# Optimization experiments

Hardware: AMD Instinct MI355X
Metric: run time of the kernel (lower is better)

Reference implementation:

```python
import jax, jax.numpy as jnp
import numpy as np

B, S, E, H = 2, 2048, 1024, 16
D = E // H


def setup_inputs() -> dict:
    key = jax.random.key(0)
    ks = jax.random.split(key, 8)
    q = jax.random.normal(ks[0], (B, S, E), dtype=jnp.float32)
    k = jax.random.normal(ks[1], (B, S, E), dtype=jnp.float32)
    v = jax.random.normal(ks[2], (B, S, E), dtype=jnp.float32)
    mask = jax.random.randint(ks[3], (B, 1, 1, S), 0, 2, dtype=jnp.int32)
    sc = 1.0 / np.sqrt(E)
    W_qkv = jax.random.normal(ks[4], (3 * E, E), dtype=jnp.float32) * sc
    b_qkv = jnp.zeros((3 * E,), dtype=jnp.float32)
    W_out = jax.random.normal(ks[5], (E, E), dtype=jnp.float32) * sc
    b_out = jnp.zeros((E,), dtype=jnp.float32)
    return {"q": q, "k": k, "v": v, "mask": mask,
            "W_qkv": W_qkv, "b_qkv": b_qkv, "W_out": W_out, "b_out": b_out}


def reference(q, k, v, mask, W_qkv, b_qkv, W_out, b_out):
    # Fused qkv linear: q takes the Q-slice, k the K-slice, v the V-slice.
    qp = (q @ W_qkv[:E].T + b_qkv[:E]).reshape(B, S, H, D)
    kp = (k @ W_qkv[E:2 * E].T + b_qkv[E:2 * E]).reshape(B, S, H, D)
    vp = (v @ W_qkv[2 * E:].T + b_qkv[2 * E:]).reshape(B, S, H, D)
    # (B,H,S,S) scores -- NOTE: original module does NOT scale by sqrt(d)
    energy = jnp.einsum('nqhd,nkhd->nhqk', qp, kp)
    energy = jnp.where(mask == 0, jnp.float32(-1e20), energy)
    attention = jax.nn.softmax(energy, axis=-1)
    out = jnp.einsum('nhql,nlhd->nqhd', attention, vp).reshape(B, S, E)
    return out @ W_out.T + b_out
```

## Files before the change

### kernel.cpp

```cpp
#include <hip/hip_runtime.h>
#include <stdint.h>

constexpr int B_ = 2, S_ = 2048, E_ = 1024, H_ = 16, D_ = 64;
constexpr int M_ = B_ * S_;

typedef unsigned short u16;
typedef __attribute__((ext_vector_type(8))) short short8;
typedef __attribute__((ext_vector_type(4))) float f32x4;

__device__ __forceinline__ u16 f2bf(float f) {
  uint32_t u = __float_as_uint(f);
  return (u16)((u + 0x7FFFu + ((u >> 16) & 1u)) >> 16);
}
__device__ __forceinline__ void tsplit(float x, u16& hi, u16& lo) {
  const uint32_t u = __float_as_uint(x);
  hi = (u16)(u >> 16);
  const float hif = __uint_as_float(u & 0xFFFF0000u);
  lo = (u16)(__float_as_uint(x - hif) >> 16);
}

typedef const __attribute__((address_space(1))) unsigned int GU32;
typedef __attribute__((address_space(3))) unsigned int LU32;
__device__ __forceinline__ void gload16(const void* g, void* l) {
  __builtin_amdgcn_global_load_lds((GU32*)g, (LU32*)l, 16, 0, 0);
}

__global__ __launch_bounds__(256) void split_f32_kernel(
    const float* __restrict__ src, u16* __restrict__ hi, u16* __restrict__ lo, int n4)
{
  const int i = blockIdx.x * 256 + threadIdx.x;
  if (i >= n4) return;
  const float4 x = ((const float4*)src)[i];
  ushort4 h, l;
  tsplit(x.x, h.x, l.x); tsplit(x.y, h.y, l.y);
  tsplit(x.z, h.z, l.z); tsplit(x.w, h.w, l.w);
  ((ushort4*)hi)[i] = h;
  ((ushort4*)lo)[i] = l;
}

__global__ __launch_bounds__(256) void mask_scan_kernel(
    const int* __restrict__ mask, int* __restrict__ opos, int* __restrict__ nk)
{
  __shared__ int tmp[256];
  __shared__ int coff;
  const int b = blockIdx.x, t = threadIdx.x;
  for (int c = t; c < S_; c += 256) opos[b * S_ + c] = 0;
  if (t == 0) coff = 0;
  __syncthreads();
  for (int c = 0; c < S_; c += 256) {
    const int m = (mask[b * S_ + c + t] != 0) ? 1 : 0;
    int x = m;
    tmp[t] = x;
    __syncthreads();
#pragma unroll
    for (int off = 1; off < 256; off <<= 1) {
      const int v = (t >= off) ? tmp[t - off] : 0;
      __syncthreads();
      x += v;
      tmp[t] = x;
      __syncthreads();
    }
    const int base = coff;
    if (m) opos[b * S_ + base + x - 1] = c + t;
    __syncthreads();
    if (t == 255) coff = base + x;
    __syncthreads();
  }
  if (t == 0) nk[b] = coff;
}

__global__ __launch_bounds__(256) void gemm_qkv_kernel(
    const float* __restrict__ q, const float* __restrict__ k, const float* __restrict__ v,
    const u16* __restrict__ WHi, const u16* __restrict__ WLo,
    const float* __restrict__ bias,
    const int* __restrict__ Opos, const int* __restrict__ NkArr,
    u16* __restrict__ QpHi, u16* __restrict__ QpLo,
    u16* __restrict__ KpHi, u16* __restrict__ KpLo,
    u16* __restrict__ Vp)
{
  __shared__ __align__(16) short smem[18432];
  float* Af = (float*)smem;
  short* Bh = smem + 8192;
  short* Bl = smem + 12288;

  const int t = threadIdx.x;
  const int m0 = blockIdx.x * 128;
  const int n0g = blockIdx.y * 128;
  const int proj = n0g >> 10;
  const int nloc = n0g & (E_ - 1);
  const bool split = (proj < 2);
  const int bb = m0 >> 11, mloc = m0 & (S_ - 1);
  const int nkb = NkArr[bb];
  if (proj != 0 && mloc >= nkb) return;

  const float* A = (proj == 0) ? q : (proj == 1) ? k : v;

  const int w = t >> 6, lane = t & 63;
  const int g = lane >> 4, lc = lane & 15;
  const int wm = w & 1, wn = w >> 1;

  const int lchA = (lane & 7) ^ (lane >> 3);
  const float* Asrc[4];
#pragma unroll
  for (int i = 0; i < 4; ++i) {
    const int r = (i * 4 + w) * 8 + (lane >> 3);
    int ga;
    if (proj == 0) ga = m0 + r;
    else ga = bb * S_ + (Opos[bb * S_ + mloc + r] & (S_ - 1));
    Asrc[i] = A + (size_t)ga * E_ + 4 * lchA;
  }
  auto gloadB = [&](int k0) {
#pragma unroll
    for (int i = 0; i < 2; ++i) {
      const int c = (w * 2 + i) * 64 + lane;
      const int row = c >> 2;
      const int sub = (c & 3) ^ ((row >> 1) & 3);
      const size_t go = (size_t)(n0g + row) * E_ + k0 + sub * 8;
      gload16(WHi + go, (char*)Bh + (w * 2 + i) * 1024);
      if (split) gload16(WLo + go, (char*)Bl + (w * 2 + i) * 1024);
    }
  };

  f32x4 acc[4][4];
#pragma unroll
  for (int i = 0; i < 4; ++i)
#pragma unroll
    for (int j = 0; j < 4; ++j) acc[i][j] = (f32x4){0.f, 0.f, 0.f, 0.f};

  for (int k0 = 0; k0 < E_; k0 += 32) {
    __syncthreads();
#pragma unroll
    for (int i = 0; i < 4; ++i)
      gload16(Asrc[i] + k0, (char*)Af + (i * 4 + w) * 1024);
    gloadB(k0);
    __syncthreads();

    short8 ah[4], al[4], bh[4], bl[4];
#pragma unroll
    for (int mt = 0; mt < 4; ++mt) {
      const int R = wm * 64 + mt * 16 + lc;
      const int s = lc & 7;
      const float4 f0 = *(const float4*)&Af[R * 32 + ((2 * g) ^ s) * 4];
      const float4 f1 = *(const float4*)&Af[R * 32 + ((2 * g + 1) ^ s) * 4];
      const float xs[8] = {f0.x, f0.y, f0.z, f0.w, f1.x, f1.y, f1.z, f1.w};
      ushort hh[8], ll[8];
#pragma unroll
      for (int j = 0; j < 8; ++j) tsplit(xs[j], hh[j], ll[j]);
      ah[mt] = *(const short8*)&hh[0];
      if (split) al[mt] = *(const short8*)&ll[0];
    }
#pragma unroll
    for (int nt = 0; nt < 4; ++nt) {
      const int row = wn * 64 + nt * 16 + lc;
      const int ro = row * 32 + ((g ^ ((row >> 1) & 3)) * 8);
      bh[nt] = *(const short8*)&Bh[ro];
      if (split) bl[nt] = *(const short8*)&Bl[ro];
    }
#pragma unroll
    for (int mt = 0; mt < 4; ++mt)
#pragma unroll
      for (int nt = 0; nt < 4; ++nt) {
        f32x4 a = acc[mt][nt];
        a = __builtin_amdgcn_mfma_f32_16x16x32_bf16(ah[mt], bh[nt], a, 0, 0, 0);
        if (split) {
          a = __builtin_amdgcn_mfma_f32_16x16x32_bf16(ah[mt], bl[nt], a, 0, 0, 0);
          a = __builtin_amdgcn_mfma_f32_16x16x32_bf16(al[mt], bh[nt], a, 0, 0, 0);
        }
        acc[mt][nt] = a;
      }
  }

  float bs[4];
#pragma unroll
  for (int nt = 0; nt < 4; ++nt) bs[nt] = bias[n0g + wn * 64 + nt * 16 + lc];

  if (proj < 2) {
    u16* Hi = (proj == 0) ? QpHi : KpHi;
    u16* Lo = (proj == 0) ? QpLo : KpLo;
    const int hwave = (nloc + wn * 64) >> 6;
    short* T = smem + w * 4608;
    const int srow_out = (proj == 0) ? ((m0 + wm * 64 + lane) & (S_ - 1))
                                     : (mloc + wm * 64 + lane);
    const size_t rowb = (((size_t)(bb * H_ + hwave)) * S_ + srow_out) * D_;
#pragma unroll
    for (int pass = 0; pass < 2; ++pass) {
      __syncthreads();
#pragma unroll
      for (int nt = 0; nt < 4; ++nt)
#pragma unroll
        for (int mt = 0; mt < 4; ++mt)
#pragma unroll
          for (int r = 0; r < 4; ++r) {
            const float val = acc[mt][nt][r] + bs[nt];
            const uint32_t u = __float_as_uint(val);
            u16 x;
            if (pass == 0) x = (u16)(u >> 16);
            else {
              const float hif = __uint_as_float(u & 0xFFFF0000u);
              x = (u16)(__float_as_uint(val - hif) >> 16);
            }
            T[(mt * 16 + g * 4 + r) * 72 + nt * 16 + lc] = (short)x;
          }
      __syncthreads();
      u16* dst = (pass == 0) ? Hi : Lo;
#pragma unroll
      for (int j = 0; j < 8; ++j)
        *(short8*)&dst[rowb + 8 * j] = *(const short8*)&T[lane * 72 + 8 * j];
    }
  } else {
#pragma unroll
    for (int mt = 0; mt < 4; ++mt) {
      const int jb = mloc + wm * 64 + mt * 16 + g * 4;
#pragma unroll
      for (int nt = 0; nt < 4; ++nt) {
        const int nE = nloc + wn * 64 + nt * 16 + lc;
        const int h = nE >> 6, d = nE & 63;
        const size_t rb = (((size_t)(bb * H_ + h)) * D_ + d) * S_;
#pragma unroll
        for (int r = 0; r < 4; ++r) {
          if (jb + r < nkb) Vp[rb + jb + r] = f2bf(acc[mt][nt][r] + bs[nt]);
        }
      }
    }
  }
}

__global__ __launch_bounds__(256, 4) void attn_mfma_kernel(
    const u16* __restrict__ QpHi, const u16* __restrict__ QpLo,
    const u16* __restrict__ KpHi, const u16* __restrict__ KpLo,
    const u16* __restrict__ Vp,
    const int* __restrict__ nkArr,
    u16* __restrict__ AOHi)
{
  __shared__ __align__(16) short sm[16896];
  short* Khi = sm;
  short* Klo = sm + 4096;
  short* Vt  = sm + 8192;
  short* Pb  = sm + 12288;

  const int t = threadIdx.x;
  const int w = t >> 6, lane = t & 63;
  const int g = lane >> 4, lc = lane & 15;
  const int bh = blockIdx.y;
  const int b = bh >> 4, hh = bh & 15;
  const int q0 = blockIdx.x * 64;
  const size_t hb = (size_t)bh * S_ * D_;
  const u16* QgH = QpHi + hb;
  const u16* QgL = QpLo + hb;
  const u16* KgH = KpHi + hb;
  const u16* KgL = KpLo + hb;
  const u16* Vg  = Vp + hb;
  short* Pw = Pb + w * 1152;

  const int nk = nkArr[b];
  const int kend = ((nk + 63) >> 6) << 6;

  short8 qh[2], ql[2];
  {
    const size_t base = (size_t)(q0 + 16 * w + lc) * D_ + 8 * g;
    qh[0] = *(const short8*)&QgH[base];
    qh[1] = *(const short8*)&QgH[base + 32];
    ql[0] = *(const short8*)&QgL[base];
    ql[1] = *(const short8*)&QgL[base + 32];
  }

  short8 ones8 = {0, 0, 0, 0, 0, 0, 0, 0};
  if (lc == 0) {
    const short o = (short)0x3F80;
    ones8 = (short8){o, o, o, o, o, o, o, o};
  }

  f32x4 O[4];
  f32x4 Ol = (f32x4){0.f, 0.f, 0.f, 0.f};
#pragma unroll
  for (int dt = 0; dt < 4; ++dt) O[dt] = (f32x4){0.f, 0.f, 0.f, 0.f};
  float mst[4] = {-INFINITY, -INFINITY, -INFINITY, -INFINITY};

  const int lch = (lane & 7) ^ (lane >> 3);
  int grow[2];
#pragma unroll
  for (int i = 0; i < 2; ++i) grow[i] = (i * 4 + w) * 8 + (lane >> 3);

  for (int kt = 0; kt < kend; kt += 64) {
    __syncthreads();
#pragma unroll
    for (int i = 0; i < 2; ++i) {
      const int row = grow[i];
      const size_t ko = (size_t)(kt + row) * D_ + lch * 8;
      gload16(KgH + ko, (char*)Khi + (i * 4 + w) * 1024);
      gload16(KgL + ko, (char*)Klo + (i * 4 + w) * 1024);
      gload16(Vg + (size_t)row * S_ + kt + lch * 8,
              (char*)Vt + (i * 4 + w) * 1024);
    }
    __syncthreads();

    f32x4 sc[4];
#pragma unroll
    for (int kt16 = 0; kt16 < 4; ++kt16) {
      const int R = 16 * kt16 + lc;
      const int s = lc & 7;
      const int o0 = R * 64 + ((g ^ s)) * 8;
      const int o1 = R * 64 + (((g + 4) ^ s)) * 8;
      const short8 kh0 = *(const short8*)&Khi[o0];
      const short8 kh1 = *(const short8*)&Khi[o1];
      const short8 kl0 = *(const short8*)&Klo[o0];
      const short8 kl1 = *(const short8*)&Klo[o1];
      f32x4 a = {0.f, 0.f, 0.f, 0.f};
      a = __builtin_amdgcn_mfma_f32_16x16x32_bf16(qh[0], kh0, a, 0, 0, 0);
      a = __builtin_amdgcn_mfma_f32_16x16x32_bf16(qh[1], kh1, a, 0, 0, 0);
      a = __builtin_amdgcn_mfma_f32_16x16x32_bf16(qh[0], kl0, a, 0, 0, 0);
      a = __builtin_amdgcn_mfma_f32_16x16x32_bf16(qh[1], kl1, a, 0, 0, 0);
      a = __builtin_amdgcn_mfma_f32_16x16x32_bf16(ql[0], kh0, a, 0, 0, 0);
      a = __builtin_amdgcn_mfma_f32_16x16x32_bf16(ql[1], kh1, a, 0, 0, 0);
      sc[kt16] = a;
    }

    if (kt + 64 > nk) {
#pragma unroll
      for (int kt16 = 0; kt16 < 4; ++kt16) {
        if (kt + 16 * kt16 + lc >= nk) {
          sc[kt16][0] = -1e20f; sc[kt16][1] = -1e20f;
          sc[kt16][2] = -1e20f; sc[kt16][3] = -1e20f;
        }
      }
    }

    float al[4];
#pragma unroll
    for (int r = 0; r < 4; ++r) {
      float vv = fmaxf(fmaxf(sc[0][r], sc[1][r]), fmaxf(sc[2][r], sc[3][r]));
      vv = fmaxf(vv, __shfl_xor(vv, 1));
      vv = fmaxf(vv, __shfl_xor(vv, 2));
      vv = fmaxf(vv, __shfl_xor(vv, 4));
      vv = fmaxf(vv, __shfl_xor(vv, 8));
      const float mn = fmaxf(mst[r], vv);
      al[r] = __expf(mst[r] - mn);
      mst[r] = mn;
    }
#pragma unroll
    for (int kt16 = 0; kt16 < 4; ++kt16) {
#pragma unroll
      for (int r = 0; r < 4; ++r)
        sc[kt16][r] = __expf(sc[kt16][r] - mst[r]);
    }
    const f32x4 alv = {al[0], al[1], al[2], al[3]};
    O[0] *= alv; O[1] *= alv; O[2] *= alv; O[3] *= alv;
    Ol *= alv;
#pragma unroll
    for (int kt16 = 0; kt16 < 4; ++kt16) {
#pragma unroll
      for (int r = 0; r < 4; ++r)
        Pw[(4 * g + r) * 72 + 16 * kt16 + lc] = (short)f2bf(sc[kt16][r]);
    }

    short8 pa[2];
    pa[0] = *(const short8*)&Pw[lc * 72 + 8 * g];
    pa[1] = *(const short8*)&Pw[lc * 72 + 32 + 8 * g];
    Ol = __builtin_amdgcn_mfma_f32_16x16x32_bf16(pa[0], ones8, Ol, 0, 0, 0);
    Ol = __builtin_amdgcn_mfma_f32_16x16x32_bf16(pa[1], ones8, Ol, 0, 0, 0);
#pragma unroll
    for (int dt = 0; dt < 4; ++dt) {
      const int R = 16 * dt + lc;
      const int s = lc & 7;
      const short8 vb0 = *(const short8*)&Vt[R * 64 + ((g ^ s)) * 8];
      const short8 vb1 = *(const short8*)&Vt[R * 64 + (((g + 4) ^ s)) * 8];
      O[dt] = __builtin_amdgcn_mfma_f32_16x16x32_bf16(pa[0], vb0, O[dt], 0, 0, 0);
      O[dt] = __builtin_amdgcn_mfma_f32_16x16x32_bf16(pa[1], vb1, O[dt], 0, 0, 0);
    }
  }

#pragma unroll
  for (int r = 0; r < 4; ++r) {
    const float lv = __shfl(Ol[r], lane & 48);
    const float lir = 1.0f / lv;
    const int qrow = q0 + 16 * w + 4 * g + r;
    const size_t rowb = (size_t)(b * S_ + qrow) * E_ + hh * 64;
#pragma unroll
    for (int dt = 0; dt < 4; ++dt)
      AOHi[rowb + dt * 16 + lc] = f2bf(O[dt][r] * lir);
  }
}

__global__ __launch_bounds__(256) void gemm_out_kernel(
    const u16* __restrict__ AHi,
    const u16* __restrict__ WHi,
    const float* __restrict__ bias, float* __restrict__ out)
{
  __shared__ __align__(16) short smem[6144];
  short* Ah = smem;
  short* Bh = smem + 2048;

  const int t = threadIdx.x;
  const int m0 = blockIdx.x * 64;
  const int n0 = blockIdx.y * 128;
  const int w = t >> 6, lane = t & 63;
  const int g = lane >> 4, lc = lane & 15;
  const int wm = w & 1, wn = w >> 1;

  f32x4 acc[2][4];
#pragma unroll
  for (int i = 0; i < 2; ++i)
#pragma unroll
    for (int j = 0; j < 4; ++j) acc[i][j] = (f32x4){0.f, 0.f, 0.f, 0.f};

  for (int k0 = 0; k0 < E_; k0 += 32) {
    {
      const int cA = w * 64 + lane;
      const int rowA = cA >> 2;
      const int subA = (cA & 3) ^ ((rowA >> 1) & 3);
      gload16(AHi + (size_t)(m0 + rowA) * E_ + k0 + subA * 8,
              (char*)Ah + w * 1024);
#pragma unroll
      for (int i = 0; i < 2; ++i) {
        const int c = (w * 2 + i) * 64 + lane;
        const int row = c >> 2;
        const int sub = (c & 3) ^ ((row >> 1) & 3);
        gload16(WHi + (size_t)(n0 + row) * E_ + k0 + sub * 8,
                (char*)Bh + (w * 2 + i) * 1024);
      }
    }
    __syncthreads();

    short8 ah[2], bh[4];
#pragma unroll
    for (int mt = 0; mt < 2; ++mt) {
      const int row = wm * 32 + mt * 16 + lc;
      ah[mt] = *(const short8*)&Ah[row * 32 + ((g ^ ((row >> 1) & 3)) * 8)];
    }
#pragma unroll
    for (int nt = 0; nt < 4; ++nt) {
      const int row = wn * 64 + nt * 16 + lc;
      bh[nt] = *(const short8*)&Bh[row * 32 + ((g ^ ((row >> 1) & 3)) * 8)];
    }
#pragma unroll
    for (int mt = 0; mt < 2; ++mt)
#pragma unroll
      for (int nt = 0; nt < 4; ++nt)
        acc[mt][nt] = __builtin_amdgcn_mfma_f32_16x16x32_bf16(ah[mt], bh[nt], acc[mt][nt], 0, 0, 0);
    __syncthreads();
  }

  float bs[4];
#pragma unroll
  for (int nt = 0; nt < 4; ++nt) bs[nt] = bias[n0 + wn * 64 + nt * 16 + lc];
#pragma unroll
  for (int nt = 0; nt < 4; ++nt) {
    const int nc = n0 + wn * 64 + nt * 16 + lc;
#pragma unroll
    for (int mt = 0; mt < 2; ++mt) {
#pragma unroll
      for (int r = 0; r < 4; ++r) {
        const int mrow = m0 + wm * 32 + mt * 16 + g * 4 + r;
        out[(size_t)mrow * E_ + nc] = acc[mt][nt][r] + bs[nt];
      }
    }
  }
}

extern "C" void kernel_launch(void* const* d_in, const int* in_sizes, int n_in,
                              void* d_out, int out_size, void* d_ws, size_t ws_size,
                              hipStream_t stream) {
  const float* q    = (const float*)d_in[0];
  const float* k    = (const float*)d_in[1];
  const float* v    = (const float*)d_in[2];
  const int*   mask = (const int*)d_in[3];
  const float* Wqkv = (const float*)d_in[4];
  const float* bqkv = (const float*)d_in[5];
  const float* Wout = (const float*)d_in[6];
  const float* bout = (const float*)d_in[7];
  float* out = (float*)d_out;

  char* wsb = (char*)d_ws;
  u16* WqkvHi = (u16*)(wsb + 0);
  u16* WqkvLo = (u16*)(wsb + 6291456);
  u16* WoutHi = (u16*)(wsb + 12582912);
  int* Opos   = (int*)(wsb + 14680064);
  int* Nk     = (int*)(wsb + 14680064 + 16384);
  u16* WoutLo = (u16*)(wsb + 14680064);
  u16* QpHi   = (u16*)(wsb + 16777216);
  u16* QpLo   = (u16*)(wsb + 25165824);
  u16* KpHi   = (u16*)(wsb + 33554432);
  u16* KpLo   = (u16*)(wsb + 41943040);
  u16* Vp     = (u16*)(wsb + 50331648);
  u16* AOHi   = (u16*)(wsb + 58720256);

  hipLaunchKernelGGL(split_f32_kernel, dim3(3072), dim3(256), 0, stream,
                     Wqkv, WqkvHi, WqkvLo, 786432);
  hipLaunchKernelGGL(split_f32_kernel, dim3(1024), dim3(256), 0, stream,
                     Wout, WoutHi, WoutLo, 262144);
  hipLaunchKernelGGL(mask_scan_kernel, dim3(B_), dim3(256), 0, stream,
                     mask, Opos, Nk);
  hipMemsetAsync(Vp, 0, 8388608, stream);
  hipLaunchKernelGGL(gemm_qkv_kernel, dim3(M_ / 128, 24), dim3(256), 0, stream,
                     q, k, v, WqkvHi, WqkvLo, bqkv, Opos, Nk,
                     QpHi, QpLo, KpHi, KpLo, Vp);
  hipLaunchKernelGGL(attn_mfma_kernel, dim3(S_ / 64, B_ * H_), dim3(256), 0, stream,
                     QpHi, QpLo, KpHi, KpLo, Vp, Nk, AOHi);
  hipLaunchKernelGGL(gemm_out_kernel, dim3(M_ / 64, E_ / 128), dim3(256), 0, stream,
                     AOHi, WoutHi, bout, out);
}
```

Baseline: 308.0 us.

## Double-buffer QKV GEMM with register-staged bf16 split and XCD-aware block remap

The QKV GEMM now prefetches the next A tile into registers and B into a second LDS buffer while computing the current one. The hi/lo bf16 split of A moves from once per wave at fragment-read time to once per element when the tile is written to LDS. This removes one barrier per k-step and the redundant split work. All three kernels also remap block IDs so that consecutive workgroups, which are dispatched round-robin across the 8 XCDs, share tiles within an XCD for L2 reuse. In exchange, the QKV kernel's LDS use doubles, which may lower occupancy.

```diff
diff --git a/kernel.cpp b/kernel.cpp
--- a/kernel.cpp
+++ b/kernel.cpp
@@ -78,14 +78,13 @@
     u16* __restrict__ KpHi, u16* __restrict__ KpLo,
     u16* __restrict__ Vp)
 {
-  __shared__ __align__(16) short smem[18432];
-  float* Af = (float*)smem;
-  short* Bh = smem + 8192;
-  short* Bl = smem + 12288;
+  __shared__ __align__(16) short smem[36864];
 
   const int t = threadIdx.x;
-  const int m0 = blockIdx.x * 128;
-  const int n0g = blockIdx.y * 128;
+  const int pl = blockIdx.x + 32 * blockIdx.y;
+  const int wg = (pl & 7) * 96 + (pl >> 3);
+  const int m0 = (wg & 31) * 128;
+  const int n0g = (wg >> 5) * 128;
   const int proj = n0g >> 10;
   const int nloc = n0g & (E_ - 1);
   const bool split = (proj < 2);
@@ -98,18 +97,40 @@
   const int w = t >> 6, lane = t & 63;
   const int g = lane >> 4, lc = lane & 15;
   const int wm = w & 1, wn = w >> 1;
-
-  const int lchA = (lane & 7) ^ (lane >> 3);
-  const float* Asrc[4];
-#pragma unroll
-  for (int i = 0; i < 4; ++i) {
-    const int r = (i * 4 + w) * 8 + (lane >> 3);
-    int ga;
-    if (proj == 0) ga = m0 + r;
-    else ga = bb * S_ + (Opos[bb * S_ + mloc + r] & (S_ - 1));
-    Asrc[i] = A + (size_t)ga * E_ + 4 * lchA;
-  }
-  auto gloadB = [&](int k0) {
+  const int sra = t >> 1, sca = (t & 1) * 16;
+
+  int arow;
+  if (proj == 0) arow = m0 + sra;
+  else arow = bb * S_ + (Opos[bb * S_ + mloc + sra] & (S_ - 1));
+  const float* Ab = A + (size_t)arow * E_ + sca;
+
+  f32x4 acc[4][4];
+#pragma unroll
+  for (int i = 0; i < 4; ++i)
+#pragma unroll
+    for (int j = 0; j < 4; ++j) acc[i][j] = (f32x4){0.f, 0.f, 0.f, 0.f};
+
+  auto loadA = [&](float4* a, int kk) {
+#pragma unroll
+    for (int i = 0; i < 4; ++i) a[i] = *(const float4*)(Ab + kk + 4 * i);
+  };
+  auto writeA = [&](const float4* a, short* Ah, short* Al) {
+    ushort hh[16], ll[16];
+#pragma unroll
+    for (int i = 0; i < 4; ++i) {
+      tsplit(a[i].x, hh[4 * i + 0], ll[4 * i + 0]);
+      tsplit(a[i].y, hh[4 * i + 1], ll[4 * i + 1]);
+      tsplit(a[i].z, hh[4 * i + 2], ll[4 * i + 2]);
+      tsplit(a[i].w, hh[4 * i + 3], ll[4 * i + 3]);
+    }
+    *(short8*)&Ah[sra * 40 + sca]     = *(const short8*)&hh[0];
+    *(short8*)&Ah[sra * 40 + sca + 8] = *(const short8*)&hh[8];
+    if (split) {
+      *(short8*)&Al[sra * 40 + sca]     = *(const short8*)&ll[0];
+      *(short8*)&Al[sra * 40 + sca + 8] = *(const short8*)&ll[8];
+    }
+  };
+  auto gloadB = [&](int k0, short* Bh, short* Bl) {
 #pragma unroll
     for (int i = 0; i < 2; ++i) {
       const int c = (w * 2 + i) * 64 + lane;
@@ -121,40 +142,36 @@
     }
   };
 
-  f32x4 acc[4][4];
-#pragma unroll
-  for (int i = 0; i < 4; ++i)
-#pragma unroll
-    for (int j = 0; j < 4; ++j) acc[i][j] = (f32x4){0.f, 0.f, 0.f, 0.f};
+  float4 ar[4];
+  loadA(ar, 0);
+  writeA(ar, smem, smem + 5120);
+  gloadB(0, smem + 10240, smem + 14336);
+  loadA(ar, 32);
+  __syncthreads();
 
   for (int k0 = 0; k0 < E_; k0 += 32) {
-    __syncthreads();
-#pragma unroll
-    for (int i = 0; i < 4; ++i)
-      gload16(Asrc[i] + k0, (char*)Af + (i * 4 + w) * 1024);
-    gloadB(k0);
-    __syncthreads();
+    const int p = (k0 >> 5) & 1;
+    short* cb = smem + p * 18432;
+    short* nb = smem + (p ^ 1) * 18432;
+    if (k0 + 32 < E_) {
+      writeA(ar, nb, nb + 5120);
+      gloadB(k0 + 32, nb + 10240, nb + 14336);
+    }
+    if (k0 + 64 < E_) loadA(ar, k0 + 64);
 
     short8 ah[4], al[4], bh[4], bl[4];
 #pragma unroll
     for (int mt = 0; mt < 4; ++mt) {
-      const int R = wm * 64 + mt * 16 + lc;
-      const int s = lc & 7;
-      const float4 f0 = *(const float4*)&Af[R * 32 + ((2 * g) ^ s) * 4];
-      const float4 f1 = *(const float4*)&Af[R * 32 + ((2 * g + 1) ^ s) * 4];
-      const float xs[8] = {f0.x, f0.y, f0.z, f0.w, f1.x, f1.y, f1.z, f1.w};
-      ushort hh[8], ll[8];
-#pragma unroll
-      for (int j = 0; j < 8; ++j) tsplit(xs[j], hh[j], ll[j]);
-      ah[mt] = *(const short8*)&hh[0];
-      if (split) al[mt] = *(const short8*)&ll[0];
+      const int ro = (wm * 64 + mt * 16 + lc) * 40 + g * 8;
+      ah[mt] = *(const short8*)&cb[ro];
+      if (split) al[mt] = *(const short8*)&cb[5120 + ro];
     }
 #pragma unroll
     for (int nt = 0; nt < 4; ++nt) {
       const int row = wn * 64 + nt * 16 + lc;
       const int ro = row * 32 + ((g ^ ((row >> 1) & 3)) * 8);
-      bh[nt] = *(const short8*)&Bh[ro];
-      if (split) bl[nt] = *(const short8*)&Bl[ro];
+      bh[nt] = *(const short8*)&cb[10240 + ro];
+      if (split) bl[nt] = *(const short8*)&cb[14336 + ro];
     }
 #pragma unroll
     for (int mt = 0; mt < 4; ++mt)
@@ -168,6 +185,7 @@
         }
         acc[mt][nt] = a;
       }
+    __syncthreads();
   }
 
   float bs[4];
@@ -241,9 +259,11 @@
   const int t = threadIdx.x;
   const int w = t >> 6, lane = t & 63;
   const int g = lane >> 4, lc = lane & 15;
-  const int bh = blockIdx.y;
+  const int pl = blockIdx.x + 32 * blockIdx.y;
+  const int wgid = (pl & 7) * 128 + (pl >> 3);
+  const int bh = wgid >> 5;
+  const int q0 = (wgid & 31) * 64;
   const int b = bh >> 4, hh = bh & 15;
-  const int q0 = blockIdx.x * 64;
   const size_t hb = (size_t)bh * S_ * D_;
   const u16* QgH = QpHi + hb;
   const u16* QgL = QpLo + hb;
@@ -391,8 +411,10 @@
   short* Bh = smem + 2048;
 
   const int t = threadIdx.x;
-  const int m0 = blockIdx.x * 64;
-  const int n0 = blockIdx.y * 128;
+  const int pl = blockIdx.x + 64 * blockIdx.y;
+  const int wg = (pl & 7) * 64 + (pl >> 3);
+  const int m0 = (wg & 63) * 64;
+  const int n0 = (wg >> 6) * 128;
   const int w = t >> 6, lane = t & 63;
   const int g = lane >> 4, lc = lane & 15;
   const int wm = w & 1, wn = w >> 1;
```

Result: faster. 284.3 us (-7.7%).
